# Kernel optimization log

Measured on AMD Instinct MI355X. Metric: run time of the kernel, lower is better.

The kernel has to match this reference:

```python
import jax, jax.numpy as jnp
import numpy as np

B, T, D_IN = 4, 512, 4096
H, G, HD = 32, 8, 128            # num_heads, num_kv_groups, head_dim
GS = H // G                      # group_size
CACHE = 3584                     # prev cache length (uniform across batch)
S = CACHE + T                    # total kv length
ROPE_BASE = 10000.0


def _rope_tables(max_pos, head_dim):
    inv_freq = 1.0 / (ROPE_BASE ** (jnp.arange(0, head_dim, 2, dtype=jnp.float32) / head_dim))
    angles = jnp.arange(max_pos, dtype=jnp.float32)[:, None] * inv_freq[None, :]  # [S, hd/2]
    angles = jnp.concatenate([angles, angles], axis=-1)                            # [S, hd]
    return jnp.cos(angles), jnp.sin(angles)


def apply_rope(x, cos, sin, start_positions):
    # x: [B, nH, T, hd]; cos/sin: [S, hd]; start_positions: [B] int
    t = x.shape[2]
    pos = start_positions[:, None] + jnp.arange(t)       # [B, T]
    c = cos[pos][:, None, :, :]                          # [B, 1, T, hd]
    s = sin[pos][:, None, :, :]
    x1, x2 = jnp.split(x, 2, axis=-1)
    rotated = jnp.concatenate([-x2, x1], axis=-1)
    return x * c + rotated * s


def setup_inputs() -> dict:
    key = jax.random.key(0)
    ks = jax.random.split(key, 8)
    x = jax.random.normal(ks[0], (B, T, D_IN), dtype=jnp.float32)
    cos, sin = _rope_tables(S, HD)
    start_positions = jnp.full((B,), CACHE, dtype=jnp.int32)
    # causal mask over absolute positions: query i sits at CACHE+i; True = masked
    kv_pos = jnp.arange(S)[None, None, None, :]
    q_pos = (CACHE + jnp.arange(T))[None, None, :, None]
    mask = jnp.broadcast_to(kv_pos > q_pos, (B, 1, T, S))
    prev_k = jax.random.normal(ks[1], (B, G, CACHE, HD), dtype=jnp.float32)
    prev_v = jax.random.normal(ks[2], (B, G, CACHE, HD), dtype=jnp.float32)
    sc = 0.02
    q_w = jax.random.normal(ks[3], (D_IN, H * HD), dtype=jnp.float32) * sc
    k_w = jax.random.normal(ks[4], (D_IN, G * HD), dtype=jnp.float32) * sc
    v_w = jax.random.normal(ks[5], (D_IN, G * HD), dtype=jnp.float32) * sc
    o_w = jax.random.normal(ks[6], (H * HD, H * HD), dtype=jnp.float32) * sc
    return {"x": x, "mask": mask, "cos": cos, "sin": sin,
            "start_positions": start_positions, "prev_k": prev_k, "prev_v": prev_v,
            "q_w": q_w, "k_w": k_w, "v_w": v_w, "o_w": o_w}


def reference(x, mask, cos, sin, start_positions, prev_k, prev_v, q_w, k_w, v_w, o_w):
    b, t, _ = x.shape
    q = (x @ q_w).reshape(b, t, H, HD).transpose(0, 2, 1, 3)   # [B,H,T,hd]
    k = (x @ k_w).reshape(b, t, G, HD).transpose(0, 2, 1, 3)   # [B,G,T,hd]
    v = (x @ v_w).reshape(b, t, G, HD).transpose(0, 2, 1, 3)   # [B,G,T,hd]
    q = apply_rope(q, cos, sin, start_positions)
    k = apply_rope(k, cos, sin, start_positions)
    # cache concat (uniform lengths -> padded batch concat)
    k_all = jnp.concatenate([prev_k, k], axis=2)               # [B,G,S,hd]
    v_all = jnp.concatenate([prev_v, v], axis=2)
    # GQA expansion: repeat each kv group for its group of query heads
    k_rep = jnp.repeat(k_all, GS, axis=1)                      # [B,H,S,hd]
    v_rep = jnp.repeat(v_all, GS, axis=1)
    scores = jnp.einsum('bhtd,bhsd->bhts', q, k_rep)
    scores = jnp.where(mask, -jnp.inf, scores)
    attn = jax.nn.softmax(scores / jnp.sqrt(jnp.asarray(HD, x.dtype)), axis=-1)
    ctx = jnp.einsum('bhts,bhsd->bthd', attn, v_rep).reshape(b, t, H * HD)
    out = ctx @ o_w
    return out, k_all, v_all
```

## Files before the change

kernel.cpp:

```cpp
#include <hip/hip_runtime.h>

#define B_     4
#define T_     512
#define DIN    4096
#define H_     32
#define G_     8
#define HD_    128
#define S_     4096
#define CACHE_ 3584
#define M_     2048
#define NQKV   6144
#define SCALE  0.08838834764831843f
#define LOG2E  1.4426950408889634f
#define QSC    (SCALE * LOG2E)

typedef __attribute__((ext_vector_type(4)))  float  f32x4;
typedef __attribute__((ext_vector_type(16))) float  f32x16;
typedef __attribute__((ext_vector_type(8)))  short  s16x8;
typedef __attribute__((ext_vector_type(4)))  unsigned short u16x4;
typedef __attribute__((ext_vector_type(8)))  unsigned short u16x8;
typedef __attribute__((ext_vector_type(4)))  unsigned int   u32x4;
typedef unsigned short u16;
typedef unsigned int   u32;

__device__ __forceinline__ u16 f2bf(float f) {
  u32 u = __builtin_bit_cast(u32, f);
  return (u16)((u + 0x7fffu + ((u >> 16) & 1u)) >> 16);
}
__device__ __forceinline__ float bf2f(u16 h) {
  return __builtin_bit_cast(float, (u32)h << 16);
}
__device__ __forceinline__ f32x4 mfma16(s16x8 a, s16x8 b, f32x4 c) {
  return __builtin_amdgcn_mfma_f32_16x16x32_bf16(a, b, c, 0, 0, 0);
}
__device__ __forceinline__ u32 pkbf(float a, float b) {
  u32 r; asm("v_cvt_pk_bf16_f32 %0, %1, %2" : "=v"(r) : "v"(a), "v"(b)); return r;
}
__device__ __forceinline__ void gload_lds16(const void* g, void* l) {
  __builtin_amdgcn_global_load_lds((__attribute__((address_space(1))) void*)g,
                                   (__attribute__((address_space(3))) void*)l, 16, 0, 0);
}

__global__ __launch_bounds__(256) void k_cvt_x(const float* __restrict__ x, u16* __restrict__ xb) {
  size_t i = ((size_t)blockIdx.x * 256 + threadIdx.x) * 4;
  f32x4 v = *(const f32x4*)(x + i);
  u16x4 o = { f2bf(v[0]), f2bf(v[1]), f2bf(v[2]), f2bf(v[3]) };
  *(u16x4*)(xb + i) = o;
}

__global__ __launch_bounds__(256) void k_twt(const float* __restrict__ src, int ldn,
                                             u16* __restrict__ dst) {
  __shared__ float tile[64][68];
  int k0 = blockIdx.x * 64, n0 = blockIdx.y * 64;
  int t = threadIdx.x;
  int rr = t >> 4, cc = (t & 15) * 4;
#pragma unroll
  for (int p = 0; p < 4; ++p) {
    int r = p * 16 + rr;
    f32x4 v = *(const f32x4*)(src + (size_t)(k0 + r) * ldn + n0 + cc);
    tile[r][cc] = v[0]; tile[r][cc + 1] = v[1]; tile[r][cc + 2] = v[2]; tile[r][cc + 3] = v[3];
  }
  __syncthreads();
#pragma unroll
  for (int p = 0; p < 4; ++p) {
    int n = p * 16 + rr;
    u16x4 o = { f2bf(tile[cc][n]), f2bf(tile[cc + 1][n]), f2bf(tile[cc + 2][n]), f2bf(tile[cc + 3][n]) };
    *(u16x4*)(dst + (size_t)(n0 + n) * 4096 + k0 + cc) = o;
  }
}

__global__ __launch_bounds__(256) void k_prep_k(const float* __restrict__ pk,
                                                float* __restrict__ k_all, u16* __restrict__ kb) {
  int bg = blockIdx.y;
  size_t si = ((size_t)blockIdx.x * 256 + threadIdx.x) * 4;
  f32x4 v = *(const f32x4*)(pk + (size_t)bg * CACHE_ * HD_ + si);
  size_t dof = (size_t)bg * S_ * HD_ + si;
  *(f32x4*)(k_all + dof) = v;
  u16x4 o = { f2bf(v[0]), f2bf(v[1]), f2bf(v[2]), f2bf(v[3]) };
  *(u16x4*)(kb + dof) = o;
}

__global__ __launch_bounds__(256) void k_prep_v(const float* __restrict__ pv,
                                                float* __restrict__ v_all, u16* __restrict__ vt) {
  __shared__ float tile[64][132];
  int bg = blockIdx.y, s0 = blockIdx.x * 64;
  int t = threadIdx.x;
  const float* src = pv + ((size_t)bg * CACHE_ + s0) * HD_;
  float* dc = v_all + ((size_t)bg * S_ + s0) * HD_;
  int r8 = t >> 5, c4 = (t & 31) * 4;
#pragma unroll
  for (int p = 0; p < 8; ++p) {
    int r = p * 8 + r8;
    f32x4 v = *(const f32x4*)(src + (size_t)r * HD_ + c4);
    *(f32x4*)(dc + (size_t)r * HD_ + c4) = v;
    tile[r][c4] = v[0]; tile[r][c4 + 1] = v[1]; tile[r][c4 + 2] = v[2]; tile[r][c4 + 3] = v[3];
  }
  __syncthreads();
  int hr = t >> 4, s4 = (t & 15) * 4;
#pragma unroll
  for (int p = 0; p < 8; ++p) {
    int hd = p * 16 + hr;
    u16x4 o = { f2bf(tile[s4][hd]), f2bf(tile[s4 + 1][hd]), f2bf(tile[s4 + 2][hd]), f2bf(tile[s4 + 3][hd]) };
    *(u16x4*)(vt + ((size_t)bg * HD_ + hd) * S_ + s0 + s4) = o;
  }
}

template<int BM, bool OUT_F32>
__global__ __launch_bounds__(512, 1) void k_gemm2(const u16* __restrict__ A, const u16* __restrict__ Bt,
                                                  void* __restrict__ Cp, int M, int N, int K) {
  constexpr int MI = BM / 32;
  constexpr int LA = BM / 64;
  __shared__ u16 As[2 * BM * 64];
  __shared__ u16 Bs[2 * 256 * 64];
  const int tid = threadIdx.x, w = tid >> 6, lane = tid & 63;
  const int wr = w >> 2, wc = w & 3;
  const int cl = lane & 15, khi = lane >> 4;
  const int Mt = M / BM;
  const int nwg = gridDim.x;
  const int q = nwg >> 3, r8 = nwg & 7;
  const int xcd = blockIdx.x & 7, pos = blockIdx.x >> 3;
  const int wgid = (xcd < r8 ? xcd * (q + 1) : r8 * (q + 1) + (xcd - r8) * q) + pos;
  const int m0 = (wgid % Mt) * BM, n0 = (wgid / Mt) * 256;
  const int rb = tid >> 3;
  const int csw = ((tid & 7) ^ (rb & 7)) * 8;
  const u16* aS = A  + (size_t)(m0 + rb) * K + csw;
  const u16* bS = Bt + (size_t)(n0 + rb) * K + csw;
  u16* aD = As + w * 512;
  u16* bD = Bs + w * 512;
  const int ck0 = ((0 + khi) ^ (cl & 7)) * 8;
  const int ck1 = ((4 + khi) ^ (cl & 7)) * 8;
  const int NT = K >> 6;
  f32x4 acc[MI][4] = {};

#define STAGE_(buf, tt)                                                                   \
  do {                                                                                    \
    _Pragma("unroll")                                                                     \
    for (int i = 0; i < LA; ++i)                                                          \
      gload_lds16(aS + (size_t)(i * 64) * K + (size_t)(tt) * 64, aD + (buf) * (BM * 64) + i * 4096); \
    _Pragma("unroll")                                                                     \
    for (int i = 0; i < 4; ++i)                                                           \
      gload_lds16(bS + (size_t)(i * 64) * K + (size_t)(tt) * 64, bD + (buf) * (256 * 64) + i * 4096); \
  } while (0)
#define VMCNT_L_()                                                                        \
  do {                                                                                    \
    if constexpr (BM == 256) asm volatile("s_waitcnt vmcnt(8)" ::: "memory");             \
    else                     asm volatile("s_waitcnt vmcnt(6)" ::: "memory");             \
  } while (0)

  STAGE_(0, 0);
  STAGE_(1, 1);
  VMCNT_L_();
  __builtin_amdgcn_sched_barrier(0);
  __builtin_amdgcn_s_barrier();
  __builtin_amdgcn_sched_barrier(0);

  for (int t = 0; t < NT; ++t) {
    const int buf = t & 1;
    const int ab = buf * (BM * 64) + (wr * (BM / 2) + cl) * 64;
    const int bb = buf * (256 * 64) + (wc * 64 + cl) * 64;
#pragma unroll
    for (int kk = 0; kk < 2; ++kk) {
      const int ck = kk ? ck1 : ck0;
      s16x8 bf4[4], af[MI];
#pragma unroll
      for (int ni = 0; ni < 4; ++ni) bf4[ni] = *(const s16x8*)(Bs + bb + ni * 16 * 64 + ck);
#pragma unroll
      for (int mi = 0; mi < MI; ++mi) af[mi] = *(const s16x8*)(As + ab + mi * 16 * 64 + ck);
      __builtin_amdgcn_s_setprio(1);
#pragma unroll
      for (int mi = 0; mi < MI; ++mi)
#pragma unroll
        for (int ni = 0; ni < 4; ++ni)
          acc[mi][ni] = mfma16(af[mi], bf4[ni], acc[mi][ni]);
      __builtin_amdgcn_s_setprio(0);
    }
    __builtin_amdgcn_sched_barrier(0);
    __builtin_amdgcn_s_barrier();
    __builtin_amdgcn_sched_barrier(0);
    if (t + 2 < NT) STAGE_(buf, t + 2);
    VMCNT_L_();
    __builtin_amdgcn_sched_barrier(0);
    __builtin_amdgcn_s_barrier();
    __builtin_amdgcn_sched_barrier(0);
  }
#undef STAGE_
#undef VMCNT_L_
  const int rl = khi * 4;
#pragma unroll
  for (int mi = 0; mi < MI; ++mi)
#pragma unroll
    for (int ni = 0; ni < 4; ++ni) {
      int col = n0 + wc * 64 + ni * 16 + cl;
#pragma unroll
      for (int r = 0; r < 4; ++r) {
        int rw = m0 + wr * (BM / 2) + mi * 16 + rl + r;
        if (OUT_F32) ((float*)Cp)[(size_t)rw * N + col] = acc[mi][ni][r];
        else         ((u16*)Cp)[(size_t)rw * N + col]   = f2bf(acc[mi][ni][r]);
      }
    }
}

__global__ __launch_bounds__(256) void k_rope(const u16* __restrict__ qkv, const float* __restrict__ cosT,
                                              const float* __restrict__ sinT, const int* __restrict__ sp,
                                              u16* __restrict__ qr, u16* __restrict__ kb,
                                              float* __restrict__ k_all, float* __restrict__ v_all) {
  int bt = blockIdx.x;
  int b = bt >> 9, t = bt & 511;
  int pos = sp[b] + t;
  const u16* row = qkv + (size_t)bt * NQKV;
  for (int idx = threadIdx.x; idx < 2560; idx += 256) {
    int head = idx >> 6, d = idx & 63;
    float c = cosT[pos * HD_ + d], s = sinT[pos * HD_ + d];
    float x1 = bf2f(row[head * HD_ + d]);
    float x2 = bf2f(row[head * HD_ + d + 64]);
    float y1 = x1 * c - x2 * s;
    float y2 = x2 * c + x1 * s;
    if (head < 32) {
      size_t o = (((size_t)b * H_ + head) * T_ + t) * HD_ + d;
      qr[o] = f2bf(y1 * QSC); qr[o + 64] = f2bf(y2 * QSC);
    } else {
      int g = head - 32;
      size_t o = (((size_t)b * G_ + g) * S_ + CACHE_ + t) * HD_ + d;
      kb[o] = f2bf(y1); kb[o + 64] = f2bf(y2);
      k_all[o] = y1; k_all[o + 64] = y2;
    }
  }
  for (int idx = threadIdx.x; idx < 1024; idx += 256) {
    int g = idx >> 7;
    float v = bf2f(row[5120 + idx]);
    size_t o = (((size_t)b * G_ + g) * S_ + CACHE_ + t) * HD_ + (idx & 127);
    v_all[o] = v;
  }
}

__global__ __launch_bounds__(256) void k_tv_new(const u16* __restrict__ qkv, u16* __restrict__ vt) {
  __shared__ u16 tile[64][72];
  int bg = blockIdx.y;
  int b = bg >> 3, g = bg & 7;
  int tt = blockIdx.x >> 1, ht = blockIdx.x & 1;
  int t0 = tt * 64, hd0 = ht * 64;
  int t = threadIdx.x;
  int rr = t >> 3, c8 = (t & 7) * 8;
#pragma unroll
  for (int p = 0; p < 2; ++p) {
    int r = p * 32 + rr;
    *(u16x8*)(&tile[r][c8]) =
      *(const u16x8*)(qkv + (size_t)(b * T_ + t0 + r) * NQKV + 5120 + g * HD_ + hd0 + c8);
  }
  __syncthreads();
  int hr = t >> 4, s4 = (t & 15) * 4;
#pragma unroll
  for (int p = 0; p < 4; ++p) {
    int hd = p * 16 + hr;
    u16x4 o = { tile[s4][hd], tile[s4 + 1][hd], tile[s4 + 2][hd], tile[s4 + 3][hd] };
    *(u16x4*)(vt + ((size_t)bg * HD_ + hd0 + hd) * S_ + CACHE_ + t0 + s4) = o;
  }
}

__global__ __launch_bounds__(512) void k_attn(const u16* __restrict__ Q, const u16* __restrict__ Kc,
                                              const u16* __restrict__ Vt, const int* __restrict__ sp,
                                              u16* __restrict__ ctx) {
  __shared__ u16 Ks[2][64 * 128];
  __shared__ u16 Vs[2][128 * 64];
  const int xcd = blockIdx.x & 7, pos = blockIdx.x >> 3;
  const int wgid = xcd * 32 + pos;
  const int qh = wgid & 1, hq = (wgid >> 1) & 3, bg = wgid >> 3;
  const int b = bg >> 3, g = bg & 7, h = g * 4 + hq;
  const int tid = threadIdx.x, w = tid >> 6, lane = tid & 63;
  const int l31 = lane & 31, hh = lane >> 5;
  const int cache = sp[b];
  const int qbase = qh * 256;
  const int qtok = qbase + w * 32 + l31;
  const size_t kvoff = (size_t)bg * S_ * HD_;
  const u16* kp = Kc + kvoff;
  const u16* vp = Vt + kvoff;
  s16x8 qreg[8];
  {
    const u16* qb = Q + ((size_t)(b * H_ + h) * T_ + qtok) * HD_;
#pragma unroll
    for (int s = 0; s < 8; ++s) qreg[s] = *(const s16x8*)(qb + s * 16 + hh * 8);
  }
  f32x16 acc[4] = {};
  float mr = -1e30f, ls = 0.f;
  const int krow = w * 8 + (lane >> 3), kch = lane & 7;
  const int vrow = w * 16 + (lane >> 2), vch = lane & 3;
  const int kswz = (krow & 15) << 3;
  const int vswz = (vrow & 7) << 3;
  const int rdswzK = (l31 & 15) << 3;
  const int rdswzV = (l31 & 7) << 3;
  const int jm = (cache + qbase + w * 32) >> 6;
  const int jlastB = (cache + qbase + 255) >> 6;
  const int kvlim = cache + qtok;
  u16x8 rk0, rk1, rv0, rv1;
  rk0 = *(const u16x8*)(kp + (size_t)krow * HD_ + kch * 8);
  rk1 = *(const u16x8*)(kp + (size_t)krow * HD_ + (kch + 8) * 8);
  rv0 = *(const u16x8*)(vp + (size_t)vrow * S_ + vch * 8);
  rv1 = *(const u16x8*)(vp + (size_t)vrow * S_ + (vch + 4) * 8);
  *(u16x8*)(Ks[0] + krow * 128 + ((kch * 8) ^ kswz))       = rk0;
  *(u16x8*)(Ks[0] + krow * 128 + (((kch + 8) * 8) ^ kswz)) = rk1;
  *(u16x8*)(Vs[0] + vrow * 64 + ((vch * 8) ^ vswz))        = rv0;
  *(u16x8*)(Vs[0] + vrow * 64 + (((vch + 4) * 8) ^ vswz))  = rv1;
  rk0 = *(const u16x8*)(kp + (size_t)(64 + krow) * HD_ + kch * 8);
  rk1 = *(const u16x8*)(kp + (size_t)(64 + krow) * HD_ + (kch + 8) * 8);
  rv0 = *(const u16x8*)(vp + (size_t)vrow * S_ + 64 + vch * 8);
  rv1 = *(const u16x8*)(vp + (size_t)vrow * S_ + 64 + (vch + 4) * 8);
  __syncthreads();
  for (int j = 0; j <= jlastB; ++j) {
    const int buf = j & 1;
    const u16* KsB = Ks[buf];
    const u16* VsB = Vs[buf];
    u16* Ksn = Ks[buf ^ 1];
    u16* Vsn = Vs[buf ^ 1];
    f32x16 sa[2] = {};
    __builtin_amdgcn_s_setprio(1);
#pragma unroll
    for (int s = 0; s < 8; ++s) {
      s16x8 ka = *(const s16x8*)(KsB + l31 * 128 + ((s * 16 + hh * 8) ^ rdswzK));
      sa[0] = __builtin_amdgcn_mfma_f32_32x32x16_bf16(ka, qreg[s], sa[0], 0, 0, 0);
    }
#pragma unroll
    for (int s = 0; s < 8; ++s) {
      s16x8 ka = *(const s16x8*)(KsB + (32 + l31) * 128 + ((s * 16 + hh * 8) ^ rdswzK));
      sa[1] = __builtin_amdgcn_mfma_f32_32x32x16_bf16(ka, qreg[s], sa[1], 0, 0, 0);
    }
    __builtin_amdgcn_s_setprio(0);
    if (j < jlastB) {
      *(u16x8*)(Ksn + krow * 128 + ((kch * 8) ^ kswz))       = rk0;
      *(u16x8*)(Ksn + krow * 128 + (((kch + 8) * 8) ^ kswz)) = rk1;
      *(u16x8*)(Vsn + vrow * 64 + ((vch * 8) ^ vswz))        = rv0;
      *(u16x8*)(Vsn + vrow * 64 + (((vch + 4) * 8) ^ vswz))  = rv1;
    }
    if (j + 2 <= jlastB) {
      rk0 = *(const u16x8*)(kp + (size_t)((j + 2) * 64 + krow) * HD_ + kch * 8);
      rk1 = *(const u16x8*)(kp + (size_t)((j + 2) * 64 + krow) * HD_ + (kch + 8) * 8);
      rv0 = *(const u16x8*)(vp + (size_t)vrow * S_ + (j + 2) * 64 + vch * 8);
      rv1 = *(const u16x8*)(vp + (size_t)vrow * S_ + (j + 2) * 64 + (vch + 4) * 8);
    }
    if (j >= jm) {
#pragma unroll
      for (int r = 0; r < 16; ++r) {
        int kv = j * 64 + (r & 3) + 8 * (r >> 2) + 4 * hh;
        if (kv > kvlim)      sa[0][r] = -1e30f;
        if (kv + 32 > kvlim) sa[1][r] = -1e30f;
      }
    }
    float mx;
    {
      float t[16];
#pragma unroll
      for (int r = 0; r < 16; ++r) t[r] = fmaxf(sa[0][r], sa[1][r]);
#define F3_(a, b, c) fmaxf(fmaxf(a, b), c)
      float u0 = F3_(t[0], t[1], t[2]);
      float u1 = F3_(t[3], t[4], t[5]);
      float u2 = F3_(t[6], t[7], t[8]);
      float u3 = F3_(t[9], t[10], t[11]);
      float u4 = F3_(t[12], t[13], t[14]);
      float lm = fmaxf(F3_(u0, u1, u2), F3_(u3, u4, t[15]));
#undef F3_
      mx = fmaxf(lm, __shfl_xor(lm, 32));
    }
    if (__any(mx > mr + 8.f)) {
      float nm = fmaxf(mr, mx);
      float al = __builtin_amdgcn_exp2f(mr - nm);
      mr = nm; ls *= al;
#pragma unroll
      for (int r = 0; r < 16; ++r) {
        float ar = __shfl(al, (r & 3) + 8 * (r >> 2) + 4 * hh, 64);
        acc[0][r] *= ar; acc[1][r] *= ar; acc[2][r] *= ar; acc[3][r] *= ar;
      }
    }
    float rs = 0.f;
#pragma unroll
    for (int r = 0; r < 16; ++r) { sa[0][r] = __builtin_amdgcn_exp2f(sa[0][r] - mr); rs += sa[0][r]; }
#pragma unroll
    for (int r = 0; r < 16; ++r) { sa[1][r] = __builtin_amdgcn_exp2f(sa[1][r] - mr); rs += sa[1][r]; }
    rs += __shfl_xor(rs, 32);
    ls += rs;
    s16x8 pf[4];
#pragma unroll
    for (int sb = 0; sb < 2; ++sb) {
      u32 a0 = pkbf(sa[sb][0],  sa[sb][1]),  a1 = pkbf(sa[sb][2],  sa[sb][3]);
      u32 b0 = pkbf(sa[sb][4],  sa[sb][5]),  b1 = pkbf(sa[sb][6],  sa[sb][7]);
      u32 c0 = pkbf(sa[sb][8],  sa[sb][9]),  c1 = pkbf(sa[sb][10], sa[sb][11]);
      u32 d0 = pkbf(sa[sb][12], sa[sb][13]), d1 = pkbf(sa[sb][14], sa[sb][15]);
      u32 xa0 = __shfl_xor(a0, 32), xa1 = __shfl_xor(a1, 32);
      u32 xb0 = __shfl_xor(b0, 32), xb1 = __shfl_xor(b1, 32);
      u32 xc0 = __shfl_xor(c0, 32), xc1 = __shfl_xor(c1, 32);
      u32 xd0 = __shfl_xor(d0, 32), xd1 = __shfl_xor(d1, 32);
      u32x4 f0 = { hh ? xb0 : a0, hh ? xb1 : a1, hh ? b0 : xa0, hh ? b1 : xa1 };
      u32x4 f1 = { hh ? xd0 : c0, hh ? xd1 : c1, hh ? d0 : xc0, hh ? d1 : xc1 };
      pf[sb * 2]     = __builtin_bit_cast(s16x8, f0);
      pf[sb * 2 + 1] = __builtin_bit_cast(s16x8, f1);
    }
    __builtin_amdgcn_s_setprio(1);
#pragma unroll
    for (int hb = 0; hb < 4; ++hb) {
      const int vro = hb * 32 + l31;
#pragma unroll
      for (int kb = 0; kb < 4; ++kb) {
        s16x8 vb = *(const s16x8*)(VsB + vro * 64 + ((kb * 16 + hh * 8) ^ rdswzV));
        acc[hb] = __builtin_amdgcn_mfma_f32_32x32x16_bf16(pf[kb], vb, acc[hb], 0, 0, 0);
      }
    }
    __builtin_amdgcn_s_setprio(0);
    __syncthreads();
  }
  float inv = 1.0f / ls;
#pragma unroll
  for (int r = 0; r < 16; ++r) {
    int ql = (r & 3) + 8 * (r >> 2) + 4 * hh;
    float ivr = __shfl(inv, ql, 64);
    u16* cb = ctx + ((size_t)(b * T_ + qbase + w * 32 + ql)) * 4096 + h * HD_ + l31;
    cb[0]  = f2bf(acc[0][r] * ivr);
    cb[32] = f2bf(acc[1][r] * ivr);
    cb[64] = f2bf(acc[2][r] * ivr);
    cb[96] = f2bf(acc[3][r] * ivr);
  }
}

extern "C" void kernel_launch(void* const* d_in, const int* in_sizes, int n_in,
                              void* d_out, int out_size, void* d_ws, size_t ws_size,
                              hipStream_t stream) {
  const float* x      = (const float*)d_in[0];
  const float* cosT   = (const float*)d_in[2];
  const float* sinT   = (const float*)d_in[3];
  const int*   sp     = (const int*)d_in[4];
  const float* prev_k = (const float*)d_in[5];
  const float* prev_v = (const float*)d_in[6];
  const float* q_w    = (const float*)d_in[7];
  const float* k_w    = (const float*)d_in[8];
  const float* v_w    = (const float*)d_in[9];
  const float* o_w    = (const float*)d_in[10];

  float* out   = (float*)d_out;
  float* k_all = out + (size_t)B_ * T_ * H_ * HD_;
  float* v_all = k_all + (size_t)B_ * G_ * S_ * HD_;

  char* w = (char*)d_ws;
  u16* wt_qkv = (u16*)(w);
  u16* wt_o   = (u16*)(w + 50331648);
  u16* x_bf   = (u16*)(w + 83886080);
  u16* qkv_bf = (u16*)(w + 100663296);
  u16* q_rope = (u16*)(w + 125829120);
  u16* k_bf   = (u16*)(w + 142606336);
  u16* v_t    = (u16*)(w + 176160768);
  u16* ctx    = (u16*)(w + 209715200);
  if (ws_size < 226492416ull) return;

  k_cvt_x<<<8192, 256, 0, stream>>>(x, x_bf);
  k_twt<<<dim3(64, 64), 256, 0, stream>>>(q_w, 4096, wt_qkv);
  k_twt<<<dim3(64, 16), 256, 0, stream>>>(k_w, 1024, wt_qkv + (size_t)4096 * 4096);
  k_twt<<<dim3(64, 16), 256, 0, stream>>>(v_w, 1024, wt_qkv + (size_t)5120 * 4096);
  k_twt<<<dim3(64, 64), 256, 0, stream>>>(o_w, 4096, wt_o);
  k_prep_k<<<dim3(448, 32), 256, 0, stream>>>(prev_k, k_all, k_bf);
  k_prep_v<<<dim3(56, 32), 256, 0, stream>>>(prev_v, v_all, v_t);
  k_gemm2<256, false><<<192, 512, 0, stream>>>(x_bf, wt_qkv, qkv_bf, M_, NQKV, 4096);
  k_rope<<<2048, 256, 0, stream>>>(qkv_bf, cosT, sinT, sp, q_rope, k_bf, k_all, v_all);
  k_tv_new<<<dim3(16, 32), 256, 0, stream>>>(qkv_bf, v_t);
  k_attn<<<256, 512, 0, stream>>>(q_rope, k_bf, v_t, sp, ctx);
  k_gemm2<128, true><<<256, 512, 0, stream>>>(ctx, wt_o, out, M_, 4096, 4096);
}
```

Baseline: 541.3 us.

## Process two KV tiles per barrier with four-slot LDS ring in attention

```diff
diff --git a/kernel.cpp b/kernel.cpp
--- a/kernel.cpp
+++ b/kernel.cpp
@@ -260,8 +260,8 @@
 __global__ __launch_bounds__(512) void k_attn(const u16* __restrict__ Q, const u16* __restrict__ Kc,
                                               const u16* __restrict__ Vt, const int* __restrict__ sp,
                                               u16* __restrict__ ctx) {
-  __shared__ u16 Ks[2][64 * 128];
-  __shared__ u16 Vs[2][128 * 64];
+  __shared__ u16 Ks[4][64 * 128];
+  __shared__ u16 Vs[4][128 * 64];
   const int xcd = blockIdx.x & 7, pos = blockIdx.x >> 3;
   const int wgid = xcd * 32 + pos;
   const int qh = wgid & 1, hq = (wgid >> 1) & 3, bg = wgid >> 3;
@@ -289,57 +289,46 @@
   const int rdswzK = (l31 & 15) << 3;
   const int rdswzV = (l31 & 7) << 3;
   const int jm = (cache + qbase + w * 32) >> 6;
-  const int jlastB = (cache + qbase + 255) >> 6;
+  const int NT = ((cache + qbase + 255) >> 6) + 1;
   const int kvlim = cache + qtok;
-  u16x8 rk0, rk1, rv0, rv1;
-  rk0 = *(const u16x8*)(kp + (size_t)krow * HD_ + kch * 8);
-  rk1 = *(const u16x8*)(kp + (size_t)krow * HD_ + (kch + 8) * 8);
-  rv0 = *(const u16x8*)(vp + (size_t)vrow * S_ + vch * 8);
-  rv1 = *(const u16x8*)(vp + (size_t)vrow * S_ + (vch + 4) * 8);
-  *(u16x8*)(Ks[0] + krow * 128 + ((kch * 8) ^ kswz))       = rk0;
-  *(u16x8*)(Ks[0] + krow * 128 + (((kch + 8) * 8) ^ kswz)) = rk1;
-  *(u16x8*)(Vs[0] + vrow * 64 + ((vch * 8) ^ vswz))        = rv0;
-  *(u16x8*)(Vs[0] + vrow * 64 + (((vch + 4) * 8) ^ vswz))  = rv1;
-  rk0 = *(const u16x8*)(kp + (size_t)(64 + krow) * HD_ + kch * 8);
-  rk1 = *(const u16x8*)(kp + (size_t)(64 + krow) * HD_ + (kch + 8) * 8);
-  rv0 = *(const u16x8*)(vp + (size_t)vrow * S_ + 64 + vch * 8);
-  rv1 = *(const u16x8*)(vp + (size_t)vrow * S_ + 64 + (vch + 4) * 8);
-  __syncthreads();
-  for (int j = 0; j <= jlastB; ++j) {
-    const int buf = j & 1;
-    const u16* KsB = Ks[buf];
-    const u16* VsB = Vs[buf];
-    u16* Ksn = Ks[buf ^ 1];
-    u16* Vsn = Vs[buf ^ 1];
-    f32x16 sa[2] = {};
+
+  auto ldK = [&](int t, u16x8& a, u16x8& c) {
+    a = *(const u16x8*)(kp + (size_t)(t * 64 + krow) * HD_ + kch * 8);
+    c = *(const u16x8*)(kp + (size_t)(t * 64 + krow) * HD_ + (kch + 8) * 8);
+  };
+  auto ldV = [&](int t, u16x8& a, u16x8& c) {
+    a = *(const u16x8*)(vp + (size_t)vrow * S_ + t * 64 + vch * 8);
+    c = *(const u16x8*)(vp + (size_t)vrow * S_ + t * 64 + (vch + 4) * 8);
+  };
+  auto stK = [&](int slot, u16x8 a, u16x8 c) {
+    *(u16x8*)(Ks[slot] + krow * 128 + ((kch * 8) ^ kswz))       = a;
+    *(u16x8*)(Ks[slot] + krow * 128 + (((kch + 8) * 8) ^ kswz)) = c;
+  };
+  auto stV = [&](int slot, u16x8 a, u16x8 c) {
+    *(u16x8*)(Vs[slot] + vrow * 64 + ((vch * 8) ^ vswz))        = a;
+    *(u16x8*)(Vs[slot] + vrow * 64 + (((vch + 4) * 8) ^ vswz))  = c;
+  };
+  auto qk = [&](const u16* KsB, f32x16* sa) {
+    f32x16 a = {}, c = {};
     __builtin_amdgcn_s_setprio(1);
 #pragma unroll
     for (int s = 0; s < 8; ++s) {
       s16x8 ka = *(const s16x8*)(KsB + l31 * 128 + ((s * 16 + hh * 8) ^ rdswzK));
-      sa[0] = __builtin_amdgcn_mfma_f32_32x32x16_bf16(ka, qreg[s], sa[0], 0, 0, 0);
+      a = __builtin_amdgcn_mfma_f32_32x32x16_bf16(ka, qreg[s], a, 0, 0, 0);
     }
 #pragma unroll
     for (int s = 0; s < 8; ++s) {
       s16x8 ka = *(const s16x8*)(KsB + (32 + l31) * 128 + ((s * 16 + hh * 8) ^ rdswzK));
-      sa[1] = __builtin_amdgcn_mfma_f32_32x32x16_bf16(ka, qreg[s], sa[1], 0, 0, 0);
+      c = __builtin_amdgcn_mfma_f32_32x32x16_bf16(ka, qreg[s], c, 0, 0, 0);
     }
     __builtin_amdgcn_s_setprio(0);
-    if (j < jlastB) {
-      *(u16x8*)(Ksn + krow * 128 + ((kch * 8) ^ kswz))       = rk0;
-      *(u16x8*)(Ksn + krow * 128 + (((kch + 8) * 8) ^ kswz)) = rk1;
-      *(u16x8*)(Vsn + vrow * 64 + ((vch * 8) ^ vswz))        = rv0;
-      *(u16x8*)(Vsn + vrow * 64 + (((vch + 4) * 8) ^ vswz))  = rv1;
-    }
-    if (j + 2 <= jlastB) {
-      rk0 = *(const u16x8*)(kp + (size_t)((j + 2) * 64 + krow) * HD_ + kch * 8);
-      rk1 = *(const u16x8*)(kp + (size_t)((j + 2) * 64 + krow) * HD_ + (kch + 8) * 8);
-      rv0 = *(const u16x8*)(vp + (size_t)vrow * S_ + (j + 2) * 64 + vch * 8);
-      rv1 = *(const u16x8*)(vp + (size_t)vrow * S_ + (j + 2) * 64 + (vch + 4) * 8);
-    }
-    if (j >= jm) {
+    sa[0] = a; sa[1] = c;
+  };
+  auto softpv = [&](f32x16* sa, const u16* VsB, int jt) {
+    if (jt >= jm) {
 #pragma unroll
       for (int r = 0; r < 16; ++r) {
-        int kv = j * 64 + (r & 3) + 8 * (r >> 2) + 4 * hh;
+        int kv = jt * 64 + (r & 3) + 8 * (r >> 2) + 4 * hh;
         if (kv > kvlim)      sa[0][r] = -1e30f;
         if (kv + 32 > kvlim) sa[1][r] = -1e30f;
       }
@@ -369,11 +358,26 @@
         acc[0][r] *= ar; acc[1][r] *= ar; acc[2][r] *= ar; acc[3][r] *= ar;
       }
     }
-    float rs = 0.f;
-#pragma unroll
-    for (int r = 0; r < 16; ++r) { sa[0][r] = __builtin_amdgcn_exp2f(sa[0][r] - mr); rs += sa[0][r]; }
-#pragma unroll
-    for (int r = 0; r < 16; ++r) { sa[1][r] = __builtin_amdgcn_exp2f(sa[1][r] - mr); rs += sa[1][r]; }
+    float p0 = 0.f, p1 = 0.f, p2 = 0.f, p3 = 0.f, p4 = 0.f, p5 = 0.f, p6 = 0.f, p7 = 0.f;
+#pragma unroll
+    for (int r = 0; r < 16; r += 4) {
+      float e0 = __builtin_amdgcn_exp2f(sa[0][r]     - mr);
+      float e1 = __builtin_amdgcn_exp2f(sa[0][r + 1] - mr);
+      float e2 = __builtin_amdgcn_exp2f(sa[0][r + 2] - mr);
+      float e3 = __builtin_amdgcn_exp2f(sa[0][r + 3] - mr);
+      sa[0][r] = e0; sa[0][r + 1] = e1; sa[0][r + 2] = e2; sa[0][r + 3] = e3;
+      p0 += e0; p1 += e1; p2 += e2; p3 += e3;
+    }
+#pragma unroll
+    for (int r = 0; r < 16; r += 4) {
+      float e0 = __builtin_amdgcn_exp2f(sa[1][r]     - mr);
+      float e1 = __builtin_amdgcn_exp2f(sa[1][r + 1] - mr);
+      float e2 = __builtin_amdgcn_exp2f(sa[1][r + 2] - mr);
+      float e3 = __builtin_amdgcn_exp2f(sa[1][r + 3] - mr);
+      sa[1][r] = e0; sa[1][r + 1] = e1; sa[1][r + 2] = e2; sa[1][r + 3] = e3;
+      p4 += e0; p5 += e1; p6 += e2; p7 += e3;
+    }
+    float rs = ((p0 + p1) + (p2 + p3)) + ((p4 + p5) + (p6 + p7));
     rs += __shfl_xor(rs, 32);
     ls += rs;
     s16x8 pf[4];
@@ -403,7 +407,39 @@
       }
     }
     __builtin_amdgcn_s_setprio(0);
+  };
+
+  u16x8 ka0, ka1, va0, va1, kb0, kb1, vb0, vb1;
+  ldK(0, ka0, ka1); ldV(0, va0, va1);
+  stK(0, ka0, ka1); stV(0, va0, va1);
+  ldK(1, kb0, kb1); ldV(1, vb0, vb1);
+  stK(1, kb0, kb1); stV(1, vb0, vb1);
+  {
+    int c2 = (2 < NT) ? 2 : NT - 1, c3 = (3 < NT) ? 3 : NT - 1;
+    ldK(c2, ka0, ka1); ldV(c2, va0, va1);
+    ldK(c3, kb0, kb1); ldV(c3, vb0, vb1);
+  }
+  __syncthreads();
+
+  const int NP = NT >> 1;
+  f32x16 sa0[2], sa1[2];
+  for (int p = 0; p < NP; ++p) {
+    const int j0 = 2 * p, j1 = j0 + 1;
+    const int cu = (p & 1) << 1, nx = cu ^ 2;
+    qk(Ks[cu], sa0);
+    qk(Ks[cu + 1], sa1);
+    if (j0 + 2 < NT) { stK(nx, ka0, ka1);     stV(nx, va0, va1); }
+    if (j1 + 2 < NT) { stK(nx + 1, kb0, kb1); stV(nx + 1, vb0, vb1); }
+    if (j0 + 4 < NT) { ldK(j0 + 4, ka0, ka1); ldV(j0 + 4, va0, va1); }
+    if (j1 + 4 < NT) { ldK(j1 + 4, kb0, kb1); ldV(j1 + 4, vb0, vb1); }
+    softpv(sa0, Vs[cu], j0);
+    softpv(sa1, Vs[cu + 1], j1);
     __syncthreads();
+  }
+  if (NT & 1) {
+    const int cu = (NP & 1) << 1;
+    qk(Ks[cu], sa0);
+    softpv(sa0, Vs[cu], NT - 1);
   }
   float inv = 1.0f / ls;
 #pragma unroll
```

New measurement: 550.0 us. About the same (+1.6%).
